# Optimization experiments

Measured on AMD Instinct MI355X. Metric: run time of the kernel, lower is better.

Reference implementation:

```python
import jax, jax.numpy as jnp
import numpy as np

FORMULA_OH_SIZES = [20, 20, 20, 20, 20]
SPECT_BIN_N = 512


def layer_norm(x, g, b, eps=1e-5):
    m = jnp.mean(x, axis=-1, keepdims=True)
    v = jnp.var(x, axis=-1, keepdims=True)
    return (x - m) * jax.lax.rsqrt(v + eps) * g + b


def gru_cell(x, h, W_ih, W_hh, b_ih, b_hh):
    # torch.nn.GRUCell math
    gi = x @ W_ih.T + b_ih
    gh = h @ W_hh.T + b_hh
    i_r, i_z, i_n = jnp.split(gi, 3, axis=-1)
    h_r, h_z, h_n = jnp.split(gh, 3, axis=-1)
    r = jax.nn.sigmoid(i_r + h_r)
    z = jax.nn.sigmoid(i_z + h_z)
    n = jnp.tanh(i_n + r * h_n)
    return (1.0 - z) * n + z * h


def structured_one_hot(x, sizes, accum=True):
    # x: [N, len(sizes)] integer element counts -> concatenated (accumulated) one-hots
    outs = []
    for i, s in enumerate(sizes):
        v = jnp.clip(x[:, i].astype(jnp.int32), 0, s - 1)
        if accum:
            oh = (jnp.arange(s)[None, :] <= v[:, None]).astype(jnp.float32)  # thermometer
        else:
            oh = jax.nn.one_hot(v, s, dtype=jnp.float32)
        outs.append(oh)
    return jnp.concatenate(outs, axis=-1)


def setup_inputs():
    key = jax.random.key(0)
    ks = jax.random.split(key, 16)
    B, A, GF, HW, S, M = 16, 32, 128, 4, 4096, 8
    G = GF * HW                       # 512 = g_feat_in * highway_steps_n
    FE = sum(FORMULA_OH_SIZES)        # 100
    D = 512                           # internal_d
    vert_feat_in = jax.random.normal(ks[0], (B, A, GF, HW), jnp.float32)
    vert_mask_in = jnp.ones((B, A), jnp.float32)
    elem_id = jax.random.randint(ks[1], (B, A), 0, 5)
    vert_element_oh = jax.nn.one_hot(elem_id, 5, dtype=jnp.float32)
    adj_oh = jnp.zeros((B, A, A, 4), jnp.float32)  # unused by forward
    atom_subsets = jax.random.bernoulli(ks[2], 0.5, (B, S, A)).astype(jnp.float32)
    masses = jax.random.uniform(ks[3], (B, S, M), jnp.float32, 0.0, SPECT_BIN_N - 1.0)
    intens = jax.random.uniform(ks[4], (B, S, M), jnp.float32)
    atom_subsets_peaks = jnp.stack([masses, intens], axis=-1)

    def lin(k, o, i):
        return (jax.random.normal(k, (o, i), jnp.float32) / np.sqrt(i)).astype(jnp.float32)

    return dict(
        vert_feat_in=vert_feat_in, vert_mask_in=vert_mask_in,
        vert_element_oh=vert_element_oh, adj_oh=adj_oh,
        atom_subsets=atom_subsets, atom_subsets_peaks=atom_subsets_peaks,
        ln_sub_g=jnp.ones((G,), jnp.float32), ln_sub_b=jnp.zeros((G,), jnp.float32),
        W_ih=lin(ks[5], 3 * G, FE), W_hh=lin(ks[6], 3 * G, G),
        b_ih=jnp.zeros((3 * G,), jnp.float32), b_hh=jnp.zeros((3 * G,), jnp.float32),
        W1=lin(ks[7], D, G), b1=jnp.zeros((D,), jnp.float32),
        W2a=lin(ks[8], D, D), b2a=jnp.zeros((D,), jnp.float32),
        W2b=lin(ks[9], D, D), b2b=jnp.zeros((D,), jnp.float32),
        ln_pre_g=jnp.ones((D,), jnp.float32), ln_pre_b=jnp.zeros((D,), jnp.float32),
        Ws=lin(ks[10], 1, D), bs=jnp.zeros((1,), jnp.float32),
    )


def reference(vert_feat_in, vert_mask_in, vert_element_oh, adj_oh, atom_subsets,
              atom_subsets_peaks, ln_sub_g, ln_sub_b, W_ih, W_hh, b_ih, b_hh,
              W1, b1, W2a, b2a, W2b, b2b, ln_pre_g, ln_pre_b, Ws, bs):
    B, A, GF, HW = vert_feat_in.shape
    S = atom_subsets.shape[1]
    vf = vert_feat_in.reshape(B, A, GF * HW)                       # [B,A,G]
    masked_vf = vf * vert_mask_in[:, :, None]
    subs_m = atom_subsets * vert_mask_in[:, None, :]               # [B,S,A]
    swvs = jnp.einsum('bag,bsa->bsg', masked_vf, subs_m)           # [B,S,G]
    # per-subset element counts -> structured one-hot formula encoding
    counts = jnp.einsum('bae,bsa->bse', vert_element_oh, atom_subsets).astype(jnp.int32)
    pf_flat = structured_one_hot(counts.reshape(B * S, -1), FORMULA_OH_SIZES, accum=True)
    subset_size = jnp.sum(subs_m, axis=2) + 1e-4                   # [B,S]
    mean = swvs / subset_size[:, :, None]
    normed = layer_norm(mean, ln_sub_g, ln_sub_b)                  # [B,S,G]
    h = gru_cell(pf_flat, normed.reshape(B * S, -1), W_ih, W_hh, b_ih, b_hh)
    h = h.reshape(normed.shape)
    x = jax.nn.relu(h @ W1.T + b1)
    x = jax.nn.relu(x @ W2a.T + b2a)
    x = jax.nn.relu(x @ W2b.T + b2b)   # (extra F.relu in original is idempotent)
    x = layer_norm(x, ln_pre_g, ln_pre_b)
    scores = (x @ Ws.T + bs)[..., 0]                               # [B,S]
    probs = jax.nn.softmax(scores, axis=-1)
    # mass histogram: scatter intensity*prob into rounded-mass bins
    masses = atom_subsets_peaks[..., 0]                            # [B,S,M]
    intens = atom_subsets_peaks[..., 1]
    bins = jnp.clip(jnp.round(masses).astype(jnp.int32), 0, SPECT_BIN_N - 1)
    contrib = intens * probs[:, :, None]                           # [B,S,M]
    spect = jnp.zeros((B, SPECT_BIN_N), x.dtype).at[
        jnp.arange(B)[:, None], bins.reshape(B, -1)].add(contrib.reshape(B, -1))
    return (spect, probs)
```

## Files before the change

### kernel.cpp

```cpp
#include <hip/hip_runtime.h>
#include <math.h>

#define B_ 16
#define A_ 32
#define G_ 512
#define S_ 4096
#define M_ 8
#define BS_ 65536
#define KC_ 640
#define NG_ 1536

typedef _Float16 half8 __attribute__((ext_vector_type(8)));
typedef _Float16 half4v __attribute__((ext_vector_type(4)));
typedef _Float16 half2v __attribute__((ext_vector_type(2)));
typedef float floatx4 __attribute__((ext_vector_type(4)));

typedef const __attribute__((address_space(1))) void* gas_t;
typedef __attribute__((address_space(3))) void* las_t;

__device__ __forceinline__ float wave_sum_f(float v){
#pragma unroll
  for (int o = 32; o > 0; o >>= 1) v += __shfl_xor(v, o);
  return v;
}
__device__ __forceinline__ float wave_max_f(float v){
#pragma unroll
  for (int o = 32; o > 0; o >>= 1) v = fmaxf(v, __shfl_xor(v, o));
  return v;
}
__device__ __forceinline__ float sigmoidf_(float x){ return 1.f/(1.f+__expf(-x)); }
__device__ __forceinline__ float tanhf_(float x){ return 1.f - 2.f/(__expf(2.f*x)+1.f); }

__global__ __launch_bounds__(256) void k_cvt3(const float* __restrict__ s0,
                                              const float* __restrict__ s1,
                                              const float* __restrict__ s2,
                                              _Float16* __restrict__ d){
  const float* s = (blockIdx.y == 0) ? s0 : (blockIdx.y == 1) ? s1 : s2;
  int i = (blockIdx.x*256 + threadIdx.x)*4;
  if (i >= G_*G_) return;
  float4 v = *(const float4*)(s+i);
  half4v o; o[0]=(_Float16)v.x; o[1]=(_Float16)v.y; o[2]=(_Float16)v.z; o[3]=(_Float16)v.w;
  *(half4v*)(d + (size_t)blockIdx.y*G_*G_ + i) = o;
}

__global__ __launch_bounds__(64) void k_buildw(const float* __restrict__ Whh,
                                               const float* __restrict__ Wih,
                                               _Float16* __restrict__ Wcat){
  int j = blockIdx.x;
  for (int p = threadIdx.x; p < KC_; p += 64){
    float v = 0.f;
    if (p < 512) v = Whh[(size_t)j*512 + p];
    else if (p < 612) v = Wih[(size_t)j*100 + (p - 512)];
    Wcat[(size_t)j*KC_ + p] = (_Float16)v;
  }
}

__global__ __launch_bounds__(256) void k_prep_mfma(
    const float* __restrict__ vf, const float* __restrict__ mask,
    const float* __restrict__ eoh, const float* __restrict__ subs,
    const float* __restrict__ ln_g, const float* __restrict__ ln_b,
    _Float16* __restrict__ Abuf){
  __shared__ _Float16 s_mvfT[G_*A_];
  __shared__ _Float16 s_sm[128*A_];
  __shared__ float s_m[A_];
  __shared__ float s_e[A_*5];
  __shared__ float s_ssum[128];
  __shared__ float s_red1[2][4][16];
  __shared__ float s_red2[2][4][16];
  int tid = threadIdx.x;
  int bx = blockIdx.x, b = blockIdx.y;
  int lane = tid & 63, w = tid >> 6;
  int q = lane >> 4, l15 = lane & 15;
  size_t row0 = (size_t)b*S_ + (size_t)bx*128;
  if (tid < A_)   s_m[tid] = mask[b*A_ + tid];
  if (tid < A_*5) s_e[tid] = eoh[b*A_*5 + tid];
  __syncthreads();
  {
    int p = tid & 15, gseg = tid >> 4;
    float mk0 = s_m[2*p], mk1 = s_m[2*p+1];
    const float* v0 = vf + ((size_t)b*A_ + 2*p)*G_ + gseg*32;
    const float* v1 = v0 + G_;
#pragma unroll
    for (int i = 0; i < 32; i += 4){
      float4 a = *(const float4*)(v0 + i);
      float4 c = *(const float4*)(v1 + i);
      float av[4] = {a.x, a.y, a.z, a.w};
      float cv[4] = {c.x, c.y, c.z, c.w};
#pragma unroll
      for (int j = 0; j < 4; ++j){
        half2v h; h[0] = (_Float16)(av[j]*mk0); h[1] = (_Float16)(cv[j]*mk1);
        *(half2v*)(s_mvfT + (gseg*32 + i + j)*A_ + 2*p) = h;
      }
    }
  }
  {
    int s = tid >> 1, hh = tid & 1;
    const float* sp = subs + (row0 + s)*A_ + hh*16;
    _Float16* dst = s_sm + s*A_ + hh*16;
#pragma unroll
    for (int i = 0; i < 16; i += 4){
      float4 v = *(const float4*)(sp + i);
      half4v h; h[0]=(_Float16)v.x; h[1]=(_Float16)v.y; h[2]=(_Float16)v.z; h[3]=(_Float16)v.w;
      *(half4v*)(dst + i) = h;
    }
  }
  __syncthreads();
  if (tid < 128){
    int s = tid;
    float ssum = 0.f, c0=0.f, c1=0.f, c2=0.f, c3=0.f, c4=0.f;
#pragma unroll
    for (int a = 0; a < A_; ++a){
      float v = (float)s_sm[s*A_ + a];
      ssum += v * s_m[a];
      c0 += v * s_e[a*5+0]; c1 += v * s_e[a*5+1]; c2 += v * s_e[a*5+2];
      c3 += v * s_e[a*5+3]; c4 += v * s_e[a*5+4];
    }
    int cc[5];
    cc[0] = min(max((int)(c0+0.5f),0),19); cc[1] = min(max((int)(c1+0.5f),0),19);
    cc[2] = min(max((int)(c2+0.5f),0),19); cc[3] = min(max((int)(c3+0.5f),0),19);
    cc[4] = min(max((int)(c4+0.5f),0),19);
    s_ssum[s] = ssum;
    _Float16* dst = Abuf + (row0 + s)*KC_ + 512;
#pragma unroll
    for (int t = 0; t < 16; ++t){
      half8 hv;
#pragma unroll
      for (int u = 0; u < 8; ++u){
        int k = t*8 + u;
        float v = 0.f;
        if (k < 100){ int f = k/20, l = k - f*20; v = (l <= cc[f]) ? 1.f : 0.f; }
        hv[u] = (_Float16)v;
      }
      *(half8*)(dst + t*8) = hv;
    }
  }
  half8 bf[8]; float lng[8], lnb[8];
#pragma unroll
  for (int t = 0; t < 8; ++t){
    int g = w*128 + t*16 + l15;
    bf[t] = *(const half8*)(s_mvfT + g*A_ + q*8);
    lng[t] = ln_g[g]; lnb[t] = ln_b[g];
  }
  __syncthreads();
  for (int gi = 0; gi < 8; ++gi){
    half8 af = *(const half8*)(s_sm + (gi*16 + l15)*A_ + q*8);
    floatx4 c[8];
#pragma unroll
    for (int t = 0; t < 8; ++t){
      floatx4 z = {0.f, 0.f, 0.f, 0.f};
      c[t] = __builtin_amdgcn_mfma_f32_16x16x32_f16(af, bf[t], z, 0, 0, 0);
    }
    float p1[4] = {0.f,0.f,0.f,0.f}, p2[4] = {0.f,0.f,0.f,0.f};
#pragma unroll
    for (int t = 0; t < 8; ++t)
#pragma unroll
      for (int r = 0; r < 4; ++r){ float v = c[t][r]; p1[r] += v; p2[r] += v*v; }
#pragma unroll
    for (int off = 1; off < 16; off <<= 1)
#pragma unroll
      for (int r = 0; r < 4; ++r){
        p1[r] += __shfl_xor(p1[r], off);
        p2[r] += __shfl_xor(p2[r], off);
      }
    int gb = gi & 1;
    if (l15 == 0){
#pragma unroll
      for (int r = 0; r < 4; ++r){ s_red1[gb][w][q*4+r] = p1[r]; s_red2[gb][w][q*4+r] = p2[r]; }
    }
    __syncthreads();
#pragma unroll
    for (int r = 0; r < 4; ++r){
      int sl = gi*16 + q*4 + r;
      int rr = q*4 + r;
      float t1 = s_red1[gb][0][rr] + s_red1[gb][1][rr] + s_red1[gb][2][rr] + s_red1[gb][3][rr];
      float t2 = s_red2[gb][0][rr] + s_red2[gb][1][rr] + s_red2[gb][2][rr] + s_red2[gb][3][rr];
      float inv = 1.f/(s_ssum[sl] + 1e-4f);
      float mu = t1*inv*(1.f/512.f);
      float var = t2*inv*inv*(1.f/512.f) - mu*mu;
      float rs = rsqrtf(var + 1e-5f);
      _Float16* orow = Abuf + (row0 + sl)*KC_;
#pragma unroll
      for (int t = 0; t < 8; ++t){
        float o = (c[t][r]*inv - mu)*rs*lng[t] + lnb[t];
        orow[w*128 + t*16 + l15] = (_Float16)o;
      }
    }
  }
}

__global__ __launch_bounds__(512) void k_gru_fused(
    const _Float16* __restrict__ Abuf, const _Float16* __restrict__ Wcat,
    const float* __restrict__ bih, const float* __restrict__ bhh,
    _Float16* __restrict__ H){
  __shared__ _Float16 smA[2][128*32];
  __shared__ _Float16 smB[2][192*32];
  int tid = threadIdx.x;
  int lane = tid & 63, wvid = tid >> 6;
  int wm = wvid & 1, wn = wvid >> 1;
  int q = lane >> 4, l15 = lane & 15;
  int mt = blockIdx.x*64 + (blockIdx.y >> 3);
  int dt = blockIdx.y & 7;
  int m0 = mt*128, n0 = dt*64;
  floatx4 acc[3][4] = {};
  floatx4 accNI[4] = {};
  int offA[4], offB[3];
#pragma unroll
  for (int i = 0; i < 4; ++i){
    int r = wm*64 + i*16 + l15;
    offA[i] = (r*4 + (q ^ ((r>>2)&3)))*8;
  }
#pragma unroll
  for (int g = 0; g < 3; ++g){
    int rb = g*64 + wn*16 + l15;
    offB[g] = (rb*4 + (q ^ ((rb>>2)&3)))*8;
  }
  const _Float16* gA;
  {
    int u = wvid*64 + lane;
    int r = u >> 2, c = (u & 3) ^ ((r >> 2) & 3);
    gA = Abuf + (size_t)(m0 + r)*KC_ + c*8;
  }
  const _Float16* gB0;
  {
    int u = wvid*64 + lane;
    int rb = u >> 2, c = (u & 3) ^ ((rb >> 2) & 3);
    int grow = (rb >> 6)*512 + n0 + (rb & 63);
    gB0 = Wcat + (size_t)grow*KC_ + c*8;
  }
  const _Float16* gB1 = nullptr;
  if (wvid < 4){
    int u = (8 + wvid)*64 + lane;
    int rb = u >> 2, c = (u & 3) ^ ((rb >> 2) & 3);
    int grow = (rb >> 6)*512 + n0 + (rb & 63);
    gB1 = Wcat + (size_t)grow*KC_ + c*8;
  }
  __builtin_amdgcn_global_load_lds((gas_t)gA,  (las_t)(smA[0] + wvid*512), 16, 0, 0);
  __builtin_amdgcn_global_load_lds((gas_t)gB0, (las_t)(smB[0] + wvid*512), 16, 0, 0);
  if (wvid < 4)
    __builtin_amdgcn_global_load_lds((gas_t)gB1, (las_t)(smB[0] + (8+wvid)*512), 16, 0, 0);
  asm volatile("s_waitcnt vmcnt(0)");
  __builtin_amdgcn_s_barrier();
  const int NT = KC_/32;
  for (int t = 0; t < NT; ++t){
    int cur = t & 1;
    if (t + 1 < NT){
      int kc = (t+1)*32;
      __builtin_amdgcn_global_load_lds((gas_t)(gA + kc),  (las_t)(smA[cur^1] + wvid*512), 16, 0, 0);
      __builtin_amdgcn_global_load_lds((gas_t)(gB0 + kc), (las_t)(smB[cur^1] + wvid*512), 16, 0, 0);
      if (wvid < 4)
        __builtin_amdgcn_global_load_lds((gas_t)(gB1 + kc), (las_t)(smB[cur^1] + (8+wvid)*512), 16, 0, 0);
    }
    half8 af[4], bfv[3];
#pragma unroll
    for (int i = 0; i < 4; ++i) af[i] = *(const half8*)(smA[cur] + offA[i]);
#pragma unroll
    for (int g = 0; g < 3; ++g) bfv[g] = *(const half8*)(smB[cur] + offB[g]);
    if (t < 16){
#pragma unroll
      for (int g = 0; g < 3; ++g)
#pragma unroll
        for (int i = 0; i < 4; ++i)
          acc[g][i] = __builtin_amdgcn_mfma_f32_16x16x32_f16(af[i], bfv[g], acc[g][i], 0, 0, 0);
    } else {
#pragma unroll
      for (int i = 0; i < 4; ++i){
        acc[0][i] = __builtin_amdgcn_mfma_f32_16x16x32_f16(af[i], bfv[0], acc[0][i], 0, 0, 0);
        acc[1][i] = __builtin_amdgcn_mfma_f32_16x16x32_f16(af[i], bfv[1], acc[1][i], 0, 0, 0);
        accNI[i]  = __builtin_amdgcn_mfma_f32_16x16x32_f16(af[i], bfv[2], accNI[i], 0, 0, 0);
      }
    }
    asm volatile("s_waitcnt vmcnt(0)");
    __builtin_amdgcn_s_barrier();
  }
  int d = n0 + wn*16 + l15;
  float br  = bih[d] + bhh[d];
  float bz  = bih[512+d] + bhh[512+d];
  float bnh = bhh[1024+d];
  float bni = bih[1024+d];
#pragma unroll
  for (int i = 0; i < 4; ++i){
#pragma unroll
    for (int r = 0; r < 4; ++r){
      int m = m0 + wm*64 + i*16 + q*4 + r;
      float gr  = acc[0][i][r] + br;
      float gz  = acc[1][i][r] + bz;
      float hn  = acc[2][i][r] + bnh;
      float in_ = accNI[i][r] + bni;
      float rrv = sigmoidf_(gr);
      float zz  = sigmoidf_(gz);
      float nn  = tanhf_(in_ + rrv*hn);
      float hp  = (float)Abuf[(size_t)m*KC_ + d];
      H[(size_t)m*G_ + d] = (_Float16)((1.f-zz)*nn + zz*hp);
    }
  }
}

__global__ __launch_bounds__(256) void k_gemm(
    const _Float16* __restrict__ A, const _Float16* __restrict__ W,
    const float* __restrict__ bias, _Float16* __restrict__ Out){
  __shared__ _Float16 smA[2][128*32];
  __shared__ _Float16 smB[2][128*32];
  int tid = threadIdx.x;
  int lane = tid & 63, wvid = tid >> 6;
  int wm = wvid & 1, wn = wvid >> 1;
  int q = lane >> 4, l15 = lane & 15;
  int mt = blockIdx.x*64 + (blockIdx.y >> 2);
  int nt = blockIdx.y & 3;
  int m0 = mt*128, n0 = nt*128;
  floatx4 acc[4][4] = {};
  int offA[4], offB[4];
#pragma unroll
  for (int i = 0; i < 4; ++i){
    int r = wm*64 + i*16 + l15;
    offA[i] = (r*4 + (q ^ ((r>>2)&3)))*8;
    int rb = wn*64 + i*16 + l15;
    offB[i] = (rb*4 + (q ^ ((rb>>2)&3)))*8;
  }
  int uA[2];
  const _Float16 *gA[2], *gB[2];
#pragma unroll
  for (int t = 0; t < 2; ++t){
    int seg = wvid*2 + t;
    int u = seg*64 + lane;
    int r = u >> 2, c = (u & 3) ^ ((r >> 2) & 3);
    uA[t] = seg;
    gA[t] = A + (size_t)(m0 + r)*G_ + c*8;
    gB[t] = W + (size_t)(n0 + r)*G_ + c*8;
  }
#pragma unroll
  for (int t2 = 0; t2 < 2; ++t2){
    __builtin_amdgcn_global_load_lds((gas_t)(gA[t2]), (las_t)(smA[0] + uA[t2]*512), 16, 0, 0);
    __builtin_amdgcn_global_load_lds((gas_t)(gB[t2]), (las_t)(smB[0] + uA[t2]*512), 16, 0, 0);
  }
  asm volatile("s_waitcnt vmcnt(0)");
  __builtin_amdgcn_s_barrier();
  const int NT = G_/32;
  for (int t = 0; t < NT; ++t){
    int cur = t & 1;
    if (t + 1 < NT){
      int kc = (t+1)*32;
#pragma unroll
      for (int t2 = 0; t2 < 2; ++t2){
        __builtin_amdgcn_global_load_lds((gas_t)(gA[t2] + kc), (las_t)(smA[cur^1] + uA[t2]*512), 16, 0, 0);
        __builtin_amdgcn_global_load_lds((gas_t)(gB[t2] + kc), (las_t)(smB[cur^1] + uA[t2]*512), 16, 0, 0);
      }
    }
    half8 af[4], bfv[4];
#pragma unroll
    for (int i = 0; i < 4; ++i) af[i] = *(const half8*)(smA[cur] + offA[i]);
#pragma unroll
    for (int j = 0; j < 4; ++j) bfv[j] = *(const half8*)(smB[cur] + offB[j]);
#pragma unroll
    for (int i = 0; i < 4; ++i)
#pragma unroll
      for (int j = 0; j < 4; ++j)
        acc[i][j] = __builtin_amdgcn_mfma_f32_16x16x32_f16(af[i], bfv[j], acc[i][j], 0, 0, 0);
    asm volatile("s_waitcnt vmcnt(0)");
    __builtin_amdgcn_s_barrier();
  }
#pragma unroll
  for (int j = 0; j < 4; ++j){
    int n = n0 + wn*64 + j*16 + l15;
    float bv = bias[n];
#pragma unroll
    for (int i = 0; i < 4; ++i){
#pragma unroll
      for (int r = 0; r < 4; ++r){
        int m = m0 + wm*64 + i*16 + q*4 + r;
        Out[(size_t)m*G_ + n] = (_Float16)fmaxf(acc[i][j][r] + bv, 0.f);
      }
    }
  }
}

__global__ __launch_bounds__(256) void k_ff3_fin(
    const _Float16* __restrict__ A, const _Float16* __restrict__ W,
    const float* __restrict__ bias, const float* __restrict__ ln_pre_g,
    const float* __restrict__ Ws, float* __restrict__ Pbuf){
  __shared__ _Float16 smA[2][128*32];
  __shared__ _Float16 smB[2][128*32];
  __shared__ float sP[2][64][2][3];
  int tid = threadIdx.x;
  int lane = tid & 63, wvid = tid >> 6;
  int wm = wvid & 1, wn = wvid >> 1;
  int q = lane >> 4, l15 = lane & 15;
  int mt = blockIdx.x*64 + (blockIdx.y >> 2);
  int nt = blockIdx.y & 3;
  int m0 = mt*128, n0 = nt*128;
  floatx4 acc[4][4] = {};
  int offA[4], offB[4];
#pragma unroll
  for (int i = 0; i < 4; ++i){
    int r = wm*64 + i*16 + l15;
    offA[i] = (r*4 + (q ^ ((r>>2)&3)))*8;
    int rb = wn*64 + i*16 + l15;
    offB[i] = (rb*4 + (q ^ ((rb>>2)&3)))*8;
  }
  int uA[2];
  const _Float16 *gA[2], *gB[2];
#pragma unroll
  for (int t = 0; t < 2; ++t){
    int seg = wvid*2 + t;
    int u = seg*64 + lane;
    int r = u >> 2, c = (u & 3) ^ ((r >> 2) & 3);
    uA[t] = seg;
    gA[t] = A + (size_t)(m0 + r)*G_ + c*8;
    gB[t] = W + (size_t)(n0 + r)*G_ + c*8;
  }
#pragma unroll
  for (int t2 = 0; t2 < 2; ++t2){
    __builtin_amdgcn_global_load_lds((gas_t)(gA[t2]), (las_t)(smA[0] + uA[t2]*512), 16, 0, 0);
    __builtin_amdgcn_global_load_lds((gas_t)(gB[t2]), (las_t)(smB[0] + uA[t2]*512), 16, 0, 0);
  }
  asm volatile("s_waitcnt vmcnt(0)");
  __builtin_amdgcn_s_barrier();
  const int NT = G_/32;
  for (int t = 0; t < NT; ++t){
    int cur = t & 1;
    if (t + 1 < NT){
      int kc = (t+1)*32;
#pragma unroll
      for (int t2 = 0; t2 < 2; ++t2){
        __builtin_amdgcn_global_load_lds((gas_t)(gA[t2] + kc), (las_t)(smA[cur^1] + uA[t2]*512), 16, 0, 0);
        __builtin_amdgcn_global_load_lds((gas_t)(gB[t2] + kc), (las_t)(smB[cur^1] + uA[t2]*512), 16, 0, 0);
      }
    }
    half8 af[4], bfv[4];
#pragma unroll
    for (int i = 0; i < 4; ++i) af[i] = *(const half8*)(smA[cur] + offA[i]);
#pragma unroll
    for (int j = 0; j < 4; ++j) bfv[j] = *(const half8*)(smB[cur] + offB[j]);
#pragma unroll
    for (int i = 0; i < 4; ++i)
#pragma unroll
      for (int j = 0; j < 4; ++j)
        acc[i][j] = __builtin_amdgcn_mfma_f32_16x16x32_f16(af[i], bfv[j], acc[i][j], 0, 0, 0);
    asm volatile("s_waitcnt vmcnt(0)");
    __builtin_amdgcn_s_barrier();
  }
  float gws[4], bv4[4];
#pragma unroll
  for (int j = 0; j < 4; ++j){
    int n = n0 + wn*64 + j*16 + l15;
    gws[j] = ln_pre_g[n]*Ws[n];
    bv4[j] = bias[n];
  }
#pragma unroll
  for (int i = 0; i < 4; ++i){
#pragma unroll
    for (int r = 0; r < 4; ++r){
      float p1 = 0.f, p2 = 0.f, p3 = 0.f;
#pragma unroll
      for (int j = 0; j < 4; ++j){
        float x = fmaxf(acc[i][j][r] + bv4[j], 0.f);
        p1 += x; p2 += x*x; p3 += gws[j]*x;
      }
#pragma unroll
      for (int off = 1; off < 16; off <<= 1){
        p1 += __shfl_xor(p1, off);
        p2 += __shfl_xor(p2, off);
        p3 += __shfl_xor(p3, off);
      }
      if (l15 == 0){
        int rl = i*16 + q*4 + r;
        sP[wm][rl][wn][0] = p1; sP[wm][rl][wn][1] = p2; sP[wm][rl][wn][2] = p3;
      }
    }
  }
  __syncthreads();
  if (tid < 128){
    int wmi = tid >> 6, rl = tid & 63;
    int m = m0 + wmi*64 + rl;
    float* dst = Pbuf + ((size_t)m*4 + nt)*3;
    dst[0] = sP[wmi][rl][0][0] + sP[wmi][rl][1][0];
    dst[1] = sP[wmi][rl][0][1] + sP[wmi][rl][1][1];
    dst[2] = sP[wmi][rl][0][2] + sP[wmi][rl][1][2];
  }
}

__global__ __launch_bounds__(256) void k_score_fin(
    const float* __restrict__ Pbuf, const float* __restrict__ g,
    const float* __restrict__ bta, const float* __restrict__ Ws,
    const float* __restrict__ bs, float* __restrict__ scores,
    float* __restrict__ spect){
  __shared__ float red[8];
  int tid = threadIdx.x, lane = tid & 63, wv = tid >> 6;
  if (blockIdx.x < 32) spect[(size_t)blockIdx.x*256 + tid] = 0.f;
  int i0 = tid*2;
  float c1p = g[i0]*Ws[i0] + g[i0+1]*Ws[i0+1];
  float c2p = bta[i0]*Ws[i0] + bta[i0+1]*Ws[i0+1];
  c1p = wave_sum_f(c1p); c2p = wave_sum_f(c2p);
  if (lane == 0){ red[wv] = c1p; red[4+wv] = c2p; }
  __syncthreads();
  float c1 = red[0]+red[1]+red[2]+red[3];
  float c2 = red[4]+red[5]+red[6]+red[7] + bs[0];
  size_t row = (size_t)blockIdx.x*256 + tid;
  const float* p = Pbuf + row*12;
  float4 a  = *(const float4*)p;
  float4 b4 = *(const float4*)(p+4);
  float4 c4 = *(const float4*)(p+8);
  float P1 = a.x + a.w + b4.z + c4.y;
  float P2 = a.y + b4.x + b4.w + c4.z;
  float P3 = a.z + b4.y + c4.x + c4.w;
  float mu = P1*(1.f/512.f);
  float var = P2*(1.f/512.f) - mu*mu;
  float rs = rsqrtf(var + 1e-5f);
  scores[row] = rs*(P3 - mu*c1) + c2;
}

__global__ __launch_bounds__(256) void k_softmax(
    const float* __restrict__ scores, float* __restrict__ probs){
  __shared__ float red[4];
  int b = blockIdx.x, tid = threadIdx.x, lane = tid & 63, wv = tid >> 6;
  const float* sp = scores + (size_t)b*S_;
  float* pp = probs + (size_t)b*S_;
  float mx = -1e30f;
  for (int i = tid; i < S_; i += 256) mx = fmaxf(mx, sp[i]);
  mx = wave_max_f(mx);
  if (lane == 0) red[wv] = mx;
  __syncthreads();
  mx = fmaxf(fmaxf(red[0], red[1]), fmaxf(red[2], red[3]));
  __syncthreads();
  float sum = 0.f;
  for (int i = tid; i < S_; i += 256){
    float e = __expf(sp[i]-mx);
    pp[i] = e;
    sum += e;
  }
  sum = wave_sum_f(sum);
  if (lane == 0) red[wv] = sum;
  __syncthreads();
  sum = red[0]+red[1]+red[2]+red[3];
  float inv = 1.f/sum;
  for (int i = tid; i < S_; i += 256)
    pp[i] *= inv;
}

__global__ __launch_bounds__(256) void k_spect_p(
    const float* __restrict__ peaks, const float* __restrict__ probs,
    float* __restrict__ spect){
  __shared__ float bins[512];
  int b = blockIdx.x, chunk = blockIdx.y, tid = threadIdx.x;
  bins[tid] = 0.f; bins[tid+256] = 0.f;
  __syncthreads();
  int s0 = chunk*(S_/8);
  for (int i = tid; i < (S_/8)*M_; i += 256){
    int s = s0 + (i >> 3), m = i & 7;
    const float* pk = peaks + (((size_t)b*S_ + s)*M_ + m)*2;
    float mass = pk[0], inten = pk[1];
    float p = probs[(size_t)b*S_ + s];
    int bin = (int)rintf(mass);
    bin = min(max(bin, 0), 511);
    atomicAdd(&bins[bin], inten*p);
  }
  __syncthreads();
  atomicAdd(&spect[(size_t)b*512 + tid],       bins[tid]);
  atomicAdd(&spect[(size_t)b*512 + tid + 256], bins[tid+256]);
}

extern "C" void kernel_launch(void* const* d_in, const int* in_sizes, int n_in,
                              void* d_out, int out_size, void* d_ws, size_t ws_size,
                              hipStream_t stream) {
  const float* vf       = (const float*)d_in[0];
  const float* mask     = (const float*)d_in[1];
  const float* eoh      = (const float*)d_in[2];
  const float* subs     = (const float*)d_in[4];
  const float* peaks    = (const float*)d_in[5];
  const float* ln_sub_g = (const float*)d_in[6];
  const float* ln_sub_b = (const float*)d_in[7];
  const float* W_ih     = (const float*)d_in[8];
  const float* W_hh     = (const float*)d_in[9];
  const float* b_ih     = (const float*)d_in[10];
  const float* b_hh     = (const float*)d_in[11];
  const float* W1       = (const float*)d_in[12];
  const float* b1       = (const float*)d_in[13];
  const float* W2a      = (const float*)d_in[14];
  const float* b2a      = (const float*)d_in[15];
  const float* W2b      = (const float*)d_in[16];
  const float* b2b      = (const float*)d_in[17];
  const float* ln_pre_g = (const float*)d_in[18];
  const float* ln_pre_b = (const float*)d_in[19];
  const float* Ws       = (const float*)d_in[20];
  const float* bs       = (const float*)d_in[21];
  float* out = (float*)d_out;
  float* probs_out = out + (size_t)B_*512;

  char* w = (char*)d_ws;
  float* scores = (float*)w;     w += (size_t)BS_*4;
  float* Pbuf   = (float*)w;     w += (size_t)BS_*12*4;
  _Float16* Wcat = (_Float16*)w; w += (size_t)NG_*KC_*2;
  _Float16* W1h  = (_Float16*)w; w += (size_t)G_*G_*2;
  _Float16* W2ah = (_Float16*)w; w += (size_t)G_*G_*2;
  _Float16* W2bh = (_Float16*)w; w += (size_t)G_*G_*2;
  _Float16* Abuf = (_Float16*)w; w += (size_t)BS_*KC_*2;
  _Float16* bufh0 = (_Float16*)w;
  _Float16* bufh1 = Abuf;

  k_cvt3<<<dim3((G_*G_/4+255)/256, 3), 256, 0, stream>>>(W1, W2a, W2b, W1h);
  k_buildw<<<NG_, 64, 0, stream>>>(W_hh, W_ih, Wcat);
  k_prep_mfma<<<dim3(S_/128, B_), 256, 0, stream>>>(vf, mask, eoh, subs,
                                                    ln_sub_g, ln_sub_b, Abuf);
  k_gru_fused<<<dim3(8, 512), 512, 0, stream>>>(Abuf, Wcat, b_ih, b_hh, bufh0);
  k_gemm<<<dim3(8, 256), 256, 0, stream>>>(bufh0, W1h,  b1,  bufh1);
  k_gemm<<<dim3(8, 256), 256, 0, stream>>>(bufh1, W2ah, b2a, bufh0);
  k_ff3_fin<<<dim3(8, 256), 256, 0, stream>>>(bufh0, W2bh, b2b,
                                              ln_pre_g, Ws, Pbuf);
  k_score_fin<<<BS_/256, 256, 0, stream>>>(Pbuf, ln_pre_g, ln_pre_b, Ws, bs,
                                           scores, out);
  k_softmax<<<B_, 256, 0, stream>>>(scores, probs_out);
  k_spect_p<<<dim3(B_, 8), 256, 0, stream>>>(peaks, probs_out, out);
}
```

Measured before the change: 504.6 us.

## Rewrite FFN GEMMs as 256x256-tile, 8-wave, phase-pipelined MFMA kernels

```diff
diff --git a/kernel.cpp b/kernel.cpp
--- a/kernel.cpp
+++ b/kernel.cpp
@@ -9,6 +9,7 @@
 #define BS_ 65536
 #define KC_ 640
 #define NG_ 1536
+#define SMH 16384
 
 typedef _Float16 half8 __attribute__((ext_vector_type(8)));
 typedef _Float16 half4v __attribute__((ext_vector_type(4)));
@@ -295,165 +296,138 @@
   }
 }
 
-__global__ __launch_bounds__(256) void k_gemm(
+
+#define STG_A8(T) do{ \
+    __builtin_amdgcn_global_load_lds((gas_t)(pA0 + (T)*64),           (las_t)(&smA8[(T)&1][0] + wvid*1024),        16, 0, 0); \
+    __builtin_amdgcn_global_load_lds((gas_t)(pA1 + (T)*64),           (las_t)(&smA8[(T)&1][0] + wvid*1024 + 512),  16, 0, 0); \
+    __builtin_amdgcn_global_load_lds((gas_t)(pA0 + 128*G_ + (T)*64),  (las_t)(&smA8[(T)&1][0] + 8192 + wvid*1024), 16, 0, 0); \
+    __builtin_amdgcn_global_load_lds((gas_t)(pA1 + 128*G_ + (T)*64),  (las_t)(&smA8[(T)&1][0] + 8192 + wvid*1024 + 512), 16, 0, 0); \
+  }while(0)
+#define STG_B8(T,H) do{ \
+    __builtin_amdgcn_global_load_lds((gas_t)(pB0 + (H)*128*G_ + (T)*64), (las_t)(&smB8[(T)&1][0] + (H)*8192 + wvid*1024),       16, 0, 0); \
+    __builtin_amdgcn_global_load_lds((gas_t)(pB1 + (H)*128*G_ + (T)*64), (las_t)(&smB8[(T)&1][0] + (H)*8192 + wvid*1024 + 512), 16, 0, 0); \
+  }while(0)
+#define RD_A8(DST, T, MF0) do{ \
+    const _Float16* ba_ = &smA8[(T)&1][0]; \
+    DST[0][0] = *(const half8*)(ba_ + aoff0 + (MF0)*1024); \
+    DST[0][1] = *(const half8*)(ba_ + aoff1 + (MF0)*1024); \
+    DST[1][0] = *(const half8*)(ba_ + aoff0 + ((MF0)+1)*1024); \
+    DST[1][1] = *(const half8*)(ba_ + aoff1 + ((MF0)+1)*1024); \
+  }while(0)
+#define RD_B8(DST, T) do{ \
+    const _Float16* bb_ = &smB8[(T)&1][0]; \
+    _Pragma("unroll") \
+    for (int nf_ = 0; nf_ < 4; ++nf_){ \
+      DST[nf_][0] = *(const half8*)(bb_ + boff0 + nf_*1024); \
+      DST[nf_][1] = *(const half8*)(bb_ + boff1 + nf_*1024); \
+    } \
+  }while(0)
+#define MMQ8(AV, BV, MF0) do{ \
+    _Pragma("unroll") \
+    for (int u_ = 0; u_ < 2; ++u_) \
+    _Pragma("unroll") \
+    for (int nf_ = 0; nf_ < 4; ++nf_){ \
+      acc[(MF0)+u_][nf_] = __builtin_amdgcn_mfma_f32_16x16x32_f16(AV[u_][0], BV[nf_][0], acc[(MF0)+u_][nf_], 0, 0, 0); \
+      acc[(MF0)+u_][nf_] = __builtin_amdgcn_mfma_f32_16x16x32_f16(AV[u_][1], BV[nf_][1], acc[(MF0)+u_][nf_], 0, 0, 0); \
+    } \
+  }while(0)
+#define PH_Q0(T, BC) do{ if ((T)+1 <= 7) STG_A8((T)+1); RD_A8(a_o, T, 2); \
+    __builtin_amdgcn_s_barrier(); __builtin_amdgcn_s_setprio(1); MMQ8(a_e, BC, 0); \
+    __builtin_amdgcn_s_setprio(0); __builtin_amdgcn_s_barrier(); }while(0)
+#define PH_Q1(T, BC) do{ if ((T)+2 <= 7) STG_B8((T)+2, 0); RD_A8(a_e, T, 4); \
+    __builtin_amdgcn_s_barrier(); __builtin_amdgcn_s_setprio(1); MMQ8(a_o, BC, 2); \
+    __builtin_amdgcn_s_setprio(0); __builtin_amdgcn_s_barrier(); }while(0)
+#define PH_Q2(T, BC) do{ if ((T)+2 <= 7) STG_B8((T)+2, 1); RD_A8(a_o, T, 6); \
+    __builtin_amdgcn_s_barrier(); __builtin_amdgcn_s_setprio(1); MMQ8(a_e, BC, 4); \
+    __builtin_amdgcn_s_setprio(0); __builtin_amdgcn_s_barrier(); }while(0)
+#define PH_Q3(T, BC, BN) do{ \
+    if ((T) < 7){ \
+      if ((T) < 6) asm volatile("s_waitcnt vmcnt(4)" ::: "memory"); \
+      else         asm volatile("s_waitcnt vmcnt(0)" ::: "memory"); \
+      RD_B8(BN, (T)+1); RD_A8(a_e, (T)+1, 0); \
+    } \
+    __builtin_amdgcn_s_barrier(); __builtin_amdgcn_s_setprio(1); MMQ8(a_o, BC, 6); \
+    __builtin_amdgcn_s_setprio(0); __builtin_amdgcn_s_barrier(); }while(0)
+#define TILE8(T, BC, BN) do{ PH_Q0(T, BC); PH_Q1(T, BC); PH_Q2(T, BC); PH_Q3(T, BC, BN); }while(0)
+
+#define K8_SETUP(Amat, Wmat) \
+  int tid = threadIdx.x; \
+  int lane = tid & 63, wvid = tid >> 6; \
+  int wm = wvid & 1, wn = wvid >> 1; \
+  int q = lane >> 4, l15 = lane & 15; \
+  int x_ = l15 & 7; \
+  int bid = blockIdx.x; \
+  int wg = (bid & 7)*64 + (bid >> 3); \
+  int mt = wg >> 1, nt = wg & 1; \
+  int m0 = mt*256, n0 = nt*256; \
+  int swzlo = (q ^ (x_ & 3))*8; \
+  int aoff0 = (wm*128 + l15)*64 + ((0 ^ (x_>>2))*4)*8 + swzlo; \
+  int aoff1 = (wm*128 + l15)*64 + ((1 ^ (x_>>2))*4)*8 + swzlo; \
+  int boff0 = (wn*64 + l15)*64 + ((0 ^ (x_>>2))*4)*8 + swzlo; \
+  int boff1 = (wn*64 + l15)*64 + ((1 ^ (x_>>2))*4)*8 + swzlo; \
+  int srow = wvid*16 + (lane >> 3); \
+  int sc = ((lane & 7) ^ ((lane >> 3) & 7))*8; \
+  const _Float16* pA0 = Amat + (size_t)(m0 + srow)*G_ + sc; \
+  const _Float16* pA1 = Amat + (size_t)(m0 + srow + 8)*G_ + sc; \
+  const _Float16* pB0 = Wmat + (size_t)(n0 + srow)*G_ + sc; \
+  const _Float16* pB1 = Wmat + (size_t)(n0 + srow + 8)*G_ + sc; \
+  floatx4 acc[8][4] = {}; \
+  half8 a_e[2][2], a_o[2][2], bA[4][2], bB[4][2]; \
+  STG_A8(0); STG_B8(0,0); STG_B8(0,1); STG_B8(1,0); STG_B8(1,1); \
+  asm volatile("s_waitcnt vmcnt(4)" ::: "memory"); \
+  __builtin_amdgcn_s_barrier(); \
+  RD_B8(bA, 0); RD_A8(a_e, 0, 0); \
+  TILE8(0, bA, bB); TILE8(1, bB, bA); \
+  TILE8(2, bA, bB); TILE8(3, bB, bA); \
+  TILE8(4, bA, bB); TILE8(5, bB, bA); \
+  TILE8(6, bA, bB); TILE8(7, bB, bA);
+
+__global__ __launch_bounds__(512, 2) void k_gemm8(
     const _Float16* __restrict__ A, const _Float16* __restrict__ W,
     const float* __restrict__ bias, _Float16* __restrict__ Out){
-  __shared__ _Float16 smA[2][128*32];
-  __shared__ _Float16 smB[2][128*32];
-  int tid = threadIdx.x;
-  int lane = tid & 63, wvid = tid >> 6;
-  int wm = wvid & 1, wn = wvid >> 1;
-  int q = lane >> 4, l15 = lane & 15;
-  int mt = blockIdx.x*64 + (blockIdx.y >> 2);
-  int nt = blockIdx.y & 3;
-  int m0 = mt*128, n0 = nt*128;
-  floatx4 acc[4][4] = {};
-  int offA[4], offB[4];
-#pragma unroll
-  for (int i = 0; i < 4; ++i){
-    int r = wm*64 + i*16 + l15;
-    offA[i] = (r*4 + (q ^ ((r>>2)&3)))*8;
-    int rb = wn*64 + i*16 + l15;
-    offB[i] = (rb*4 + (q ^ ((rb>>2)&3)))*8;
-  }
-  int uA[2];
-  const _Float16 *gA[2], *gB[2];
-#pragma unroll
-  for (int t = 0; t < 2; ++t){
-    int seg = wvid*2 + t;
-    int u = seg*64 + lane;
-    int r = u >> 2, c = (u & 3) ^ ((r >> 2) & 3);
-    uA[t] = seg;
-    gA[t] = A + (size_t)(m0 + r)*G_ + c*8;
-    gB[t] = W + (size_t)(n0 + r)*G_ + c*8;
-  }
-#pragma unroll
-  for (int t2 = 0; t2 < 2; ++t2){
-    __builtin_amdgcn_global_load_lds((gas_t)(gA[t2]), (las_t)(smA[0] + uA[t2]*512), 16, 0, 0);
-    __builtin_amdgcn_global_load_lds((gas_t)(gB[t2]), (las_t)(smB[0] + uA[t2]*512), 16, 0, 0);
-  }
-  asm volatile("s_waitcnt vmcnt(0)");
-  __builtin_amdgcn_s_barrier();
-  const int NT = G_/32;
-  for (int t = 0; t < NT; ++t){
-    int cur = t & 1;
-    if (t + 1 < NT){
-      int kc = (t+1)*32;
-#pragma unroll
-      for (int t2 = 0; t2 < 2; ++t2){
-        __builtin_amdgcn_global_load_lds((gas_t)(gA[t2] + kc), (las_t)(smA[cur^1] + uA[t2]*512), 16, 0, 0);
-        __builtin_amdgcn_global_load_lds((gas_t)(gB[t2] + kc), (las_t)(smB[cur^1] + uA[t2]*512), 16, 0, 0);
-      }
-    }
-    half8 af[4], bfv[4];
-#pragma unroll
-    for (int i = 0; i < 4; ++i) af[i] = *(const half8*)(smA[cur] + offA[i]);
-#pragma unroll
-    for (int j = 0; j < 4; ++j) bfv[j] = *(const half8*)(smB[cur] + offB[j]);
-#pragma unroll
-    for (int i = 0; i < 4; ++i)
-#pragma unroll
-      for (int j = 0; j < 4; ++j)
-        acc[i][j] = __builtin_amdgcn_mfma_f32_16x16x32_f16(af[i], bfv[j], acc[i][j], 0, 0, 0);
-    asm volatile("s_waitcnt vmcnt(0)");
-    __builtin_amdgcn_s_barrier();
-  }
-#pragma unroll
-  for (int j = 0; j < 4; ++j){
-    int n = n0 + wn*64 + j*16 + l15;
-    float bv = bias[n];
-#pragma unroll
-    for (int i = 0; i < 4; ++i){
-#pragma unroll
-      for (int r = 0; r < 4; ++r){
-        int m = m0 + wm*64 + i*16 + q*4 + r;
-        Out[(size_t)m*G_ + n] = (_Float16)fmaxf(acc[i][j][r] + bv, 0.f);
-      }
-    }
-  }
-}
-
-__global__ __launch_bounds__(256) void k_ff3_fin(
+  __shared__ _Float16 smA8[2][SMH];
+  __shared__ _Float16 smB8[2][SMH];
+  K8_SETUP(A, W)
+  float bv[4];
+#pragma unroll
+  for (int nf = 0; nf < 4; ++nf) bv[nf] = bias[n0 + wn*64 + nf*16 + l15];
+#pragma unroll
+  for (int mf = 0; mf < 8; ++mf){
+    int m = m0 + wm*128 + mf*16 + q*4;
+#pragma unroll
+    for (int nf = 0; nf < 4; ++nf){
+      int n = n0 + wn*64 + nf*16 + l15;
+#pragma unroll
+      for (int r = 0; r < 4; ++r)
+        Out[(size_t)(m+r)*G_ + n] = (_Float16)fmaxf(acc[mf][nf][r] + bv[nf], 0.f);
+    }
+  }
+}
+
+__global__ __launch_bounds__(512, 2) void k_ff38(
     const _Float16* __restrict__ A, const _Float16* __restrict__ W,
     const float* __restrict__ bias, const float* __restrict__ ln_pre_g,
     const float* __restrict__ Ws, float* __restrict__ Pbuf){
-  __shared__ _Float16 smA[2][128*32];
-  __shared__ _Float16 smB[2][128*32];
-  __shared__ float sP[2][64][2][3];
-  int tid = threadIdx.x;
-  int lane = tid & 63, wvid = tid >> 6;
-  int wm = wvid & 1, wn = wvid >> 1;
-  int q = lane >> 4, l15 = lane & 15;
-  int mt = blockIdx.x*64 + (blockIdx.y >> 2);
-  int nt = blockIdx.y & 3;
-  int m0 = mt*128, n0 = nt*128;
-  floatx4 acc[4][4] = {};
-  int offA[4], offB[4];
-#pragma unroll
-  for (int i = 0; i < 4; ++i){
-    int r = wm*64 + i*16 + l15;
-    offA[i] = (r*4 + (q ^ ((r>>2)&3)))*8;
-    int rb = wn*64 + i*16 + l15;
-    offB[i] = (rb*4 + (q ^ ((rb>>2)&3)))*8;
-  }
-  int uA[2];
-  const _Float16 *gA[2], *gB[2];
-#pragma unroll
-  for (int t = 0; t < 2; ++t){
-    int seg = wvid*2 + t;
-    int u = seg*64 + lane;
-    int r = u >> 2, c = (u & 3) ^ ((r >> 2) & 3);
-    uA[t] = seg;
-    gA[t] = A + (size_t)(m0 + r)*G_ + c*8;
-    gB[t] = W + (size_t)(n0 + r)*G_ + c*8;
-  }
-#pragma unroll
-  for (int t2 = 0; t2 < 2; ++t2){
-    __builtin_amdgcn_global_load_lds((gas_t)(gA[t2]), (las_t)(smA[0] + uA[t2]*512), 16, 0, 0);
-    __builtin_amdgcn_global_load_lds((gas_t)(gB[t2]), (las_t)(smB[0] + uA[t2]*512), 16, 0, 0);
-  }
-  asm volatile("s_waitcnt vmcnt(0)");
-  __builtin_amdgcn_s_barrier();
-  const int NT = G_/32;
-  for (int t = 0; t < NT; ++t){
-    int cur = t & 1;
-    if (t + 1 < NT){
-      int kc = (t+1)*32;
-#pragma unroll
-      for (int t2 = 0; t2 < 2; ++t2){
-        __builtin_amdgcn_global_load_lds((gas_t)(gA[t2] + kc), (las_t)(smA[cur^1] + uA[t2]*512), 16, 0, 0);
-        __builtin_amdgcn_global_load_lds((gas_t)(gB[t2] + kc), (las_t)(smB[cur^1] + uA[t2]*512), 16, 0, 0);
-      }
-    }
-    half8 af[4], bfv[4];
-#pragma unroll
-    for (int i = 0; i < 4; ++i) af[i] = *(const half8*)(smA[cur] + offA[i]);
-#pragma unroll
-    for (int j = 0; j < 4; ++j) bfv[j] = *(const half8*)(smB[cur] + offB[j]);
-#pragma unroll
-    for (int i = 0; i < 4; ++i)
-#pragma unroll
-      for (int j = 0; j < 4; ++j)
-        acc[i][j] = __builtin_amdgcn_mfma_f32_16x16x32_f16(af[i], bfv[j], acc[i][j], 0, 0, 0);
-    asm volatile("s_waitcnt vmcnt(0)");
-    __builtin_amdgcn_s_barrier();
-  }
-  float gws[4], bv4[4];
-#pragma unroll
-  for (int j = 0; j < 4; ++j){
-    int n = n0 + wn*64 + j*16 + l15;
-    gws[j] = ln_pre_g[n]*Ws[n];
-    bv4[j] = bias[n];
-  }
-#pragma unroll
-  for (int i = 0; i < 4; ++i){
+  __shared__ _Float16 smA8[2][SMH];
+  __shared__ _Float16 smB8[2][SMH];
+  K8_SETUP(A, W)
+  float gws[4], bv[4];
+#pragma unroll
+  for (int nf = 0; nf < 4; ++nf){
+    int n = n0 + wn*64 + nf*16 + l15;
+    gws[nf] = ln_pre_g[n]*Ws[n];
+    bv[nf] = bias[n];
+  }
+  float* sP = (float*)&smB8[0][0];
+#pragma unroll
+  for (int mf = 0; mf < 8; ++mf){
 #pragma unroll
     for (int r = 0; r < 4; ++r){
       float p1 = 0.f, p2 = 0.f, p3 = 0.f;
 #pragma unroll
-      for (int j = 0; j < 4; ++j){
-        float x = fmaxf(acc[i][j][r] + bv4[j], 0.f);
-        p1 += x; p2 += x*x; p3 += gws[j]*x;
+      for (int nf = 0; nf < 4; ++nf){
+        float xv = fmaxf(acc[mf][nf][r] + bv[nf], 0.f);
+        p1 += xv; p2 += xv*xv; p3 += gws[nf]*xv;
       }
 #pragma unroll
       for (int off = 1; off < 16; off <<= 1){
@@ -462,19 +436,21 @@
         p3 += __shfl_xor(p3, off);
       }
       if (l15 == 0){
-        int rl = i*16 + q*4 + r;
-        sP[wm][rl][wn][0] = p1; sP[wm][rl][wn][1] = p2; sP[wm][rl][wn][2] = p3;
-      }
-    }
-  }
-  __syncthreads();
-  if (tid < 128){
-    int wmi = tid >> 6, rl = tid & 63;
-    int m = m0 + wmi*64 + rl;
-    float* dst = Pbuf + ((size_t)m*4 + nt)*3;
-    dst[0] = sP[wmi][rl][0][0] + sP[wmi][rl][1][0];
-    dst[1] = sP[wmi][rl][0][1] + sP[wmi][rl][1][1];
-    dst[2] = sP[wmi][rl][0][2] + sP[wmi][rl][1][2];
+        int rl = wm*128 + mf*16 + q*4 + r;
+        sP[(rl*4 + wn)*3 + 0] = p1;
+        sP[(rl*4 + wn)*3 + 1] = p2;
+        sP[(rl*4 + wn)*3 + 2] = p3;
+      }
+    }
+  }
+  __syncthreads();
+  if (tid < 256){
+    int m = m0 + tid;
+    float* dst = Pbuf + ((size_t)m*2 + nt)*3;
+#pragma unroll
+    for (int c = 0; c < 3; ++c)
+      dst[c] = sP[(tid*4+0)*3+c] + sP[(tid*4+1)*3+c] +
+               sP[(tid*4+2)*3+c] + sP[(tid*4+3)*3+c];
   }
 }
 
@@ -495,13 +471,13 @@
   float c1 = red[0]+red[1]+red[2]+red[3];
   float c2 = red[4]+red[5]+red[6]+red[7] + bs[0];
   size_t row = (size_t)blockIdx.x*256 + tid;
-  const float* p = Pbuf + row*12;
-  float4 a  = *(const float4*)p;
-  float4 b4 = *(const float4*)(p+4);
-  float4 c4 = *(const float4*)(p+8);
-  float P1 = a.x + a.w + b4.z + c4.y;
-  float P2 = a.y + b4.x + b4.w + c4.z;
-  float P3 = a.z + b4.y + c4.x + c4.w;
+  const float* p = Pbuf + row*6;
+  float2 u0 = *(const float2*)p;
+  float2 u1 = *(const float2*)(p+2);
+  float2 u2 = *(const float2*)(p+4);
+  float P1 = u0.x + u1.y;
+  float P2 = u0.y + u2.x;
+  float P3 = u1.x + u2.y;
   float mu = P1*(1.f/512.f);
   float var = P2*(1.f/512.f) - mu*mu;
   float rs = rsqrtf(var + 1e-5f);
@@ -601,10 +577,9 @@
   k_prep_mfma<<<dim3(S_/128, B_), 256, 0, stream>>>(vf, mask, eoh, subs,
                                                     ln_sub_g, ln_sub_b, Abuf);
   k_gru_fused<<<dim3(8, 512), 512, 0, stream>>>(Abuf, Wcat, b_ih, b_hh, bufh0);
-  k_gemm<<<dim3(8, 256), 256, 0, stream>>>(bufh0, W1h,  b1,  bufh1);
-  k_gemm<<<dim3(8, 256), 256, 0, stream>>>(bufh1, W2ah, b2a, bufh0);
-  k_ff3_fin<<<dim3(8, 256), 256, 0, stream>>>(bufh0, W2bh, b2b,
-                                              ln_pre_g, Ws, Pbuf);
+  k_gemm8<<<512, 512, 0, stream>>>(bufh0, W1h,  b1,  bufh1);
+  k_gemm8<<<512, 512, 0, stream>>>(bufh1, W2ah, b2a, bufh0);
+  k_ff38<<<512, 512, 0, stream>>>(bufh0, W2bh, b2b, ln_pre_g, Ws, Pbuf);
   k_score_fin<<<BS_/256, 256, 0, stream>>>(Pbuf, ln_pre_g, ln_pre_b, Ws, bs,
                                            scores, out);
   k_softmax<<<B_, 256, 0, stream>>>(scores, probs_out);
```

New measurement: 470.0 us. 6.9% less time.
